# Performance work log

Hardware: AMD Instinct MI355X
Metric: run time of the kernel (lower is better)

Reference implementation:

```python
import jax, jax.numpy as jnp
import numpy as np

H = 16  # heads
K_POLY = 3  # K from init


def setup_inputs() -> dict:
    key = jax.random.key(0)
    ks = jax.random.split(key, 6)
    B, N, D = 4, 1024, 1024
    s = 1.0 / np.sqrt(D)
    return {
        "x": jax.random.normal(ks[0], (B, N, D), jnp.float32),
        "Wq": jax.random.normal(ks[1], (D, D), jnp.float32) * s,
        "bq": jnp.zeros((D,), jnp.float32),
        "Wk": jax.random.normal(ks[2], (D, D), jnp.float32) * s,
        "bk": jnp.zeros((D,), jnp.float32),
        "Wv": jax.random.normal(ks[3], (D, D), jnp.float32) * s,
        "bv": jnp.zeros((D,), jnp.float32),
        "Wo": jax.random.normal(ks[4], (D, D), jnp.float32) * s,
        "bo": jnp.zeros((D,), jnp.float32),
        "w0": jnp.zeros((H,), jnp.float32),
        "w1": jnp.ones((H,), jnp.float32),
        "wK": jnp.zeros((H,), jnp.float32),
    }


def reference(x, Wq, bq, Wk, bk, Wv, bv, Wo, bo, w0, w1, wK):
    B, N, D = x.shape
    d = D // H
    # projections -> [B, H, N, d]
    def proj(W, b):
        return (x @ W + b).reshape(B, N, H, d).transpose(0, 2, 1, 3)
    q = proj(Wq, bq)
    k = proj(Wk, bk)
    v = proj(Wv, bv)
    att = jax.nn.softmax(jnp.einsum('bhnd,bhmd->bhnm', q, k) / jnp.sqrt(jnp.float32(d)), axis=-1)
    att2 = jnp.einsum('bhnm,bhmk->bhnk', att, att)  # att @ att
    attK = att + (K_POLY - 1) * (att2 - att)
    eye = jnp.eye(N, dtype=x.dtype)  # [N, N]
    gf = (w0[None, :, None, None] * eye[None, None]
          + w1[None, :, None, None] * att
          + wK[None, :, None, None] * attK)
    out = jnp.einsum('bhnm,bhmd->bhnd', gf, v)  # [B, H, N, d]
    out = out.transpose(0, 2, 1, 3).reshape(B, N, D)
    return out @ Wo + bo
```

## Files before the change

kernel.cpp:

```cpp
#include <hip/hip_runtime.h>

typedef unsigned short u16;
typedef unsigned int u32;
typedef __attribute__((ext_vector_type(8))) short short8;
typedef __attribute__((ext_vector_type(4))) float f32x4;

__device__ __forceinline__ u16 f2bf(float f) {
  union { float f; u32 u; } c; c.f = f;
  u32 u = c.u;
  u += 0x7fffu + ((u >> 16) & 1u);
  return (u16)(u >> 16);
}
__device__ __forceinline__ float bf2f(u16 h) {
  union { u32 u; float f; } c; c.u = ((u32)h) << 16;
  return c.f;
}

#define GLDS16(g, l)                                                          \
  __builtin_amdgcn_global_load_lds(                                           \
      (const __attribute__((address_space(1))) u32*)(g),                      \
      (__attribute__((address_space(3))) u32*)(l), 16, 0, 0)

#define EXP_SCALE 0.18033688011112042f

__global__ __launch_bounds__(256) void k_cast_x(const float* __restrict__ x,
                                                u16* __restrict__ xb) {
  int i = blockIdx.x * 256 + threadIdx.x;
  float4 v = ((const float4*)x)[i];
  short4 s;
  s.x = (short)f2bf(v.x); s.y = (short)f2bf(v.y);
  s.z = (short)f2bf(v.z); s.w = (short)f2bf(v.w);
  *(short4*)(xb + (size_t)i * 4) = s;
}

__global__ __launch_bounds__(256) void k_trans_w(
    const float* __restrict__ W0, const float* __restrict__ W1,
    const float* __restrict__ W2, const float* __restrict__ W3,
    u16* __restrict__ T0, u16* __restrict__ T1, u16* __restrict__ T2,
    u16* __restrict__ T3) {
  const float* W = blockIdx.z == 0 ? W0 : blockIdx.z == 1 ? W1 : blockIdx.z == 2 ? W2 : W3;
  u16* T = blockIdx.z == 0 ? T0 : blockIdx.z == 1 ? T1 : blockIdx.z == 2 ? T2 : T3;
  __shared__ float tile[32][33];
  int r0 = blockIdx.y * 32, c0 = blockIdx.x * 32;
  int tid = threadIdx.x;
  for (int i = tid; i < 1024; i += 256) {
    int r = i >> 5, c = i & 31;
    tile[r][c] = W[(size_t)(r0 + r) * 1024 + c0 + c];
  }
  __syncthreads();
  for (int i = tid; i < 1024; i += 256) {
    int r = i >> 5, c = i & 31;
    T[(size_t)(c0 + r) * 1024 + r0 + c] = f2bf(tile[c][r]);
  }
}

__global__ __launch_bounds__(512, 2) void k_proj(
    const u16* __restrict__ xb, const u16* __restrict__ WqT,
    const u16* __restrict__ WkT, const u16* __restrict__ WvT,
    const float* __restrict__ bq, const float* __restrict__ bk,
    const float* __restrict__ bv, u16* __restrict__ qh, u16* __restrict__ kh,
    u16* __restrict__ vh, u16* __restrict__ vT) {
  __shared__ __align__(16) u16 As[2][256 * 64];
  __shared__ __align__(16) u16 Bs[2][256 * 64];
  const int m0 = blockIdx.x * 256, n0 = blockIdx.y * 256;
  const int which = blockIdx.z;
  const u16* Ag = xb + (size_t)m0 * 1024;
  const u16* Bg = (which == 0 ? WqT : which == 1 ? WkT : WvT) + (size_t)n0 * 1024;
  const float* bias = which == 0 ? bq : which == 1 ? bk : bv;
  const int tid = threadIdx.x, lane = tid & 63, wid = tid >> 6;
  const int wm = wid >> 2, wn = wid & 3, fr = lane & 15, fg = lane >> 4;

  f32x4 acc[8][4];
#pragma unroll
  for (int i = 0; i < 8; ++i)
#pragma unroll
    for (int j = 0; j < 4; ++j) acc[i][j] = f32x4{0.f, 0.f, 0.f, 0.f};

  auto stage = [&](int kt, int buf) {
#pragma unroll
    for (int L = 0; L < 4; ++L) {
      int q = L * 512 + tid;
      int row = q >> 3, c = q & 7;
      int kc = c ^ (row & 7);
      GLDS16(Ag + (size_t)row * 1024 + kt * 64 + kc * 8, &As[buf][q * 8]);
    }
#pragma unroll
    for (int L = 0; L < 4; ++L) {
      int q = L * 512 + tid;
      int row = q >> 3, c = q & 7;
      int kc = c ^ (row & 7);
      GLDS16(Bg + (size_t)row * 1024 + kt * 64 + kc * 8, &Bs[buf][q * 8]);
    }
  };

  stage(0, 0);
  asm volatile("s_waitcnt vmcnt(0)" ::: "memory");
  __builtin_amdgcn_s_barrier();
  asm volatile("" ::: "memory");
  int cur = 0;
  for (int kt = 0; kt < 16; ++kt) {
    if (kt + 1 < 16) stage(kt + 1, cur ^ 1);
    const u16* as = &As[cur][0];
    const u16* bs = &Bs[cur][0];
#pragma unroll
    for (int ks = 0; ks < 2; ++ks) {
      short8 bf_[4];
#pragma unroll
      for (int j = 0; j < 4; ++j) {
        int row = wn * 64 + j * 16 + fr;
        int kk = ks * 4 + fg;
        bf_[j] = *(const short8*)(bs + row * 64 + ((kk ^ (row & 7)) * 8));
      }
#pragma unroll
      for (int mh = 0; mh < 2; ++mh) {
        short8 af_[4];
#pragma unroll
        for (int i = 0; i < 4; ++i) {
          int row = wm * 128 + mh * 64 + i * 16 + fr;
          int kk = ks * 4 + fg;
          af_[i] = *(const short8*)(as + row * 64 + ((kk ^ (row & 7)) * 8));
        }
#pragma unroll
        for (int i = 0; i < 4; ++i)
#pragma unroll
          for (int j = 0; j < 4; ++j)
            acc[mh * 4 + i][j] = __builtin_amdgcn_mfma_f32_16x16x32_bf16(
                af_[i], bf_[j], acc[mh * 4 + i][j], 0, 0, 0);
      }
    }
    asm volatile("s_waitcnt vmcnt(0) lgkmcnt(0)" ::: "memory");
    __builtin_amdgcn_s_barrier();
    asm volatile("" ::: "memory");
    cur ^= 1;
  }
#pragma unroll
  for (int f = 0; f < 8; ++f)
#pragma unroll
    for (int j2 = 0; j2 < 4; ++j2) {
      int n = n0 + wn * 64 + j2 * 16 + fr;
      float bb = bias[n];
      int h = n >> 6, dc = n & 63;
#pragma unroll
      for (int r = 0; r < 4; ++r) {
        int m = m0 + wm * 128 + (f >> 2) * 64 + (f & 3) * 16 + fg * 4 + r;
        int b = m >> 10, nr = m & 1023;
        int z = b * 16 + h;
        float val = acc[f][j2][r] + bb;
        u16 bv16 = f2bf(val);
        if (which == 0) {
          qh[((size_t)z * 1024 + nr) * 64 + dc] = bv16;
        } else if (which == 1) {
          kh[((size_t)z * 1024 + nr) * 64 + dc] = bv16;
        } else {
          vh[((size_t)z * 1024 + nr) * 64 + dc] = bv16;
          vT[((size_t)z * 64 + dc) * 1024 + nr] = bv16;
        }
      }
    }
}

__device__ __forceinline__ void core128x64_p3(const u16* __restrict__ A,
                                              const u16* __restrict__ Bt, int K,
                                              f32x4 (&acc)[2][4], u16* As,
                                              u16* Bs) {
  const int tid = threadIdx.x;
  const int lane = tid & 63;
  const int w = tid >> 6;
  const int fr = lane & 15, fg = lane >> 4;
  const int sr = tid >> 2, sc = (tid & 3) * 8;
#pragma unroll
  for (int i = 0; i < 2; ++i)
#pragma unroll
    for (int j = 0; j < 4; ++j) acc[i][j] = f32x4{0.f, 0.f, 0.f, 0.f};

  auto stage = [&](int t, int slot) {
    u16* as = As + slot * 4096;
    u16* bs = Bs + slot * 2048;
    const int k0 = t * 32 + sc;
    GLDS16(A + (size_t)sr * K + k0, as + tid * 8);
    GLDS16(A + (size_t)(sr + 64) * K + k0, as + (256 + tid) * 8);
    GLDS16(Bt + (size_t)sr * K + k0, bs + tid * 8);
  };
  auto compute = [&](int slot) {
    const u16* as = As + slot * 4096;
    const u16* bs = Bs + slot * 2048;
    short8 af[2], bfv[4];
#pragma unroll
    for (int i = 0; i < 2; ++i)
      af[i] = *(const short8*)(as + (w * 32 + i * 16 + fr) * 32 + fg * 8);
#pragma unroll
    for (int j = 0; j < 4; ++j)
      bfv[j] = *(const short8*)(bs + (j * 16 + fr) * 32 + fg * 8);
#pragma unroll
    for (int i = 0; i < 2; ++i)
#pragma unroll
      for (int j = 0; j < 4; ++j)
        acc[i][j] = __builtin_amdgcn_mfma_f32_16x16x32_bf16(af[i], bfv[j],
                                                            acc[i][j], 0, 0, 0);
  };

  const int NS = K / 32;
  stage(0, 0);
  stage(1, 1);
  int cs = 0, ss = 2;
  for (int t = 0; t + 2 < NS; ++t) {
    asm volatile("s_waitcnt vmcnt(3) lgkmcnt(0)" ::: "memory");
    __builtin_amdgcn_s_barrier();
    asm volatile("" ::: "memory");
    stage(t + 2, ss);
    compute(cs);
    cs = cs == 2 ? 0 : cs + 1;
    ss = ss == 2 ? 0 : ss + 1;
  }
  asm volatile("s_waitcnt vmcnt(3) lgkmcnt(0)" ::: "memory");
  __builtin_amdgcn_s_barrier();
  asm volatile("" ::: "memory");
  compute(cs);
  cs = cs == 2 ? 0 : cs + 1;
  asm volatile("s_waitcnt vmcnt(0) lgkmcnt(0)" ::: "memory");
  __builtin_amdgcn_s_barrier();
  asm volatile("" ::: "memory");
  compute(cs);
}

__global__ __launch_bounds__(256) void k_pass1(
    const u16* __restrict__ qh, const u16* __restrict__ kh,
    const u16* __restrict__ vT, u16* __restrict__ P1T,
    u16* __restrict__ P1h, float* __restrict__ mlinv) {
  __shared__ __align__(16) u16 Ks[64 * 64];
  __shared__ __align__(16) u16 Vs[64 * 64];
  __shared__ __align__(16) u16 Ps[4][16 * 64];
  const int li = blockIdx.x + 16 * blockIdx.y;
  const int cx = li & 7, jb = li >> 3;
  const int z = cx * 8 + (jb >> 4);
  const int m0 = (jb & 15) * 64;
  const int tid = threadIdx.x, lane = tid & 63, w = tid >> 6;
  const int fr = lane & 15, fg = lane >> 4;
  const int row0 = m0 + w * 16;
  const u16* qbase = qh + (size_t)z * 65536;
  const u16* kbase = kh + (size_t)z * 65536;
  const u16* vbase = vT + (size_t)z * 65536;
  u16* myP = &Ps[w][0];

  short8 qf[2];
#pragma unroll
  for (int kc = 0; kc < 2; ++kc)
    qf[kc] = *(const short8*)(qbase + (size_t)(row0 + fr) * 64 + (kc * 4 + fg) * 8);

  f32x4 o[4];
  float rs[4];
#pragma unroll
  for (int ct = 0; ct < 4; ++ct) o[ct] = f32x4{0.f, 0.f, 0.f, 0.f};
#pragma unroll
  for (int r = 0; r < 4; ++r) rs[r] = 0.f;

  for (int t = 0; t < 16; ++t) {
    const int kv0 = t * 64;
#pragma unroll
    for (int it = 0; it < 2; ++it) {
      int idx = it * 256 + tid;
      int row = idx >> 3, cc = idx & 7;
      GLDS16(kbase + (size_t)(kv0 + row) * 64 + ((cc ^ (row & 7)) * 8),
             Ks + idx * 8);
      GLDS16(vbase + (size_t)row * 1024 + kv0 + ((cc ^ (row & 7)) * 8),
             Vs + idx * 8);
    }
    __syncthreads();
#pragma unroll
    for (int ct = 0; ct < 4; ++ct) {
      int krow = ct * 16 + fr;
      short8 k0 = *(const short8*)(Ks + krow * 64 + ((fg ^ (krow & 7)) * 8));
      short8 k1 = *(const short8*)(Ks + krow * 64 + (((4 + fg) ^ (krow & 7)) * 8));
      f32x4 s = __builtin_amdgcn_mfma_f32_16x16x32_bf16(
          qf[0], k0, f32x4{0.f, 0.f, 0.f, 0.f}, 0, 0, 0);
      s = __builtin_amdgcn_mfma_f32_16x16x32_bf16(qf[1], k1, s, 0, 0, 0);
      int pcol = ct * 16 + fr;
      int cc = pcol >> 3;
#pragma unroll
      for (int r = 0; r < 4; ++r) {
        float e = __builtin_exp2f(s[r] * EXP_SCALE);
        rs[r] += e;
        int prow = fg * 4 + r;
        myP[prow * 64 + ((cc ^ (prow & 7)) * 8) + (pcol & 7)] = f2bf(e);
      }
    }
    asm volatile("s_waitcnt lgkmcnt(0)" ::: "memory");
    short8 p0 = *(const short8*)(myP + fr * 64 + ((fg ^ (fr & 7)) * 8));
    short8 p1 = *(const short8*)(myP + fr * 64 + (((4 + fg) ^ (fr & 7)) * 8));
#pragma unroll
    for (int ct = 0; ct < 4; ++ct) {
      int vrow = ct * 16 + fr;
      short8 v0 = *(const short8*)(Vs + vrow * 64 + ((fg ^ (vrow & 7)) * 8));
      short8 v1 = *(const short8*)(Vs + vrow * 64 + (((4 + fg) ^ (vrow & 7)) * 8));
      o[ct] = __builtin_amdgcn_mfma_f32_16x16x32_bf16(p0, v0, o[ct], 0, 0, 0);
      o[ct] = __builtin_amdgcn_mfma_f32_16x16x32_bf16(p1, v1, o[ct], 0, 0, 0);
    }
    __syncthreads();
  }
#pragma unroll
  for (int off = 1; off < 16; off <<= 1)
#pragma unroll
    for (int r = 0; r < 4; ++r) rs[r] += __shfl_xor(rs[r], off, 64);
  float linv[4];
#pragma unroll
  for (int r = 0; r < 4; ++r) linv[r] = 1.f / rs[r];
#pragma unroll
  for (int ct = 0; ct < 4; ++ct) {
    union { u16 u[4]; short4 s4; } pk;
#pragma unroll
    for (int r = 0; r < 4; ++r) {
      u16 b_ = f2bf(o[ct][r] * linv[r]);
      pk.u[r] = b_;
      myP[(fg * 4 + r) * 64 + ct * 16 + fr] = b_;
    }
    *(short4*)(P1T + ((size_t)z * 64 + ct * 16 + fr) * 1024 + row0 + fg * 4) =
        pk.s4;
  }
  asm volatile("s_waitcnt lgkmcnt(0)" ::: "memory");
  {
    int r_ = lane >> 2;
#pragma unroll
    for (int ch2 = 0; ch2 < 2; ++ch2) {
      int ch = (lane & 3) * 2 + ch2;
      int4 vv = *(const int4*)(myP + r_ * 64 + ch * 8);
      *(int4*)(P1h + ((size_t)z * 1024 + row0 + r_) * 64 + ch * 8) = vv;
    }
  }
  if (fr == 0) {
#pragma unroll
    for (int r = 0; r < 4; ++r)
      mlinv[(size_t)z * 1024 + row0 + fg * 4 + r] = linv[r];
  }
}

__global__ __launch_bounds__(256) void k_pass2(
    const u16* __restrict__ qh, const u16* __restrict__ kh,
    const u16* __restrict__ P1T, const u16* __restrict__ vh,
    const u16* __restrict__ P1h, const float* __restrict__ mlinv,
    const float* __restrict__ w0, const float* __restrict__ w1,
    const float* __restrict__ wK, u16* __restrict__ OH) {
  __shared__ __align__(16) u16 Ks[64 * 64];
  __shared__ __align__(16) u16 Ts[64 * 64];
  __shared__ __align__(16) u16 Ps[4][16 * 64];
  const int li = blockIdx.x + 16 * blockIdx.y;
  const int cx = li & 7, jb = li >> 3;
  const int z = cx * 8 + (jb >> 4);
  const int m0 = (jb & 15) * 64;
  const int tid = threadIdx.x, lane = tid & 63, w = tid >> 6;
  const int fr = lane & 15, fg = lane >> 4;
  const int row0 = m0 + w * 16;
  const int h = z & 15, b = z >> 4;
  const float cw0 = w0[h], cw1 = w1[h] - wK[h], cw2 = 2.f * wK[h];
  const u16* qbase = qh + (size_t)z * 65536;
  const u16* kbase = kh + (size_t)z * 65536;
  const u16* tbase = P1T + (size_t)z * 65536;
  u16* myP = &Ps[w][0];

  short8 qf[2];
#pragma unroll
  for (int kc = 0; kc < 2; ++kc)
    qf[kc] = *(const short8*)(qbase + (size_t)(row0 + fr) * 64 + (kc * 4 + fg) * 8);
  float lrow[4];
#pragma unroll
  for (int r = 0; r < 4; ++r)
    lrow[r] = mlinv[(size_t)z * 1024 + row0 + fg * 4 + r];
  f32x4 o[4];
#pragma unroll
  for (int ct = 0; ct < 4; ++ct) o[ct] = f32x4{0.f, 0.f, 0.f, 0.f};

  for (int t = 0; t < 16; ++t) {
    const int kv0 = t * 64;
#pragma unroll
    for (int it = 0; it < 2; ++it) {
      int idx = it * 256 + tid;
      int row = idx >> 3, cc = idx & 7;
      GLDS16(kbase + (size_t)(kv0 + row) * 64 + ((cc ^ (row & 7)) * 8),
             Ks + idx * 8);
      GLDS16(tbase + (size_t)row * 1024 + kv0 + ((cc ^ (row & 7)) * 8),
             Ts + idx * 8);
    }
    __syncthreads();
#pragma unroll
    for (int ct = 0; ct < 4; ++ct) {
      int krow = ct * 16 + fr;
      short8 k0 = *(const short8*)(Ks + krow * 64 + ((fg ^ (krow & 7)) * 8));
      short8 k1 = *(const short8*)(Ks + krow * 64 + (((4 + fg) ^ (krow & 7)) * 8));
      f32x4 s = __builtin_amdgcn_mfma_f32_16x16x32_bf16(
          qf[0], k0, f32x4{0.f, 0.f, 0.f, 0.f}, 0, 0, 0);
      s = __builtin_amdgcn_mfma_f32_16x16x32_bf16(qf[1], k1, s, 0, 0, 0);
      int pcol = ct * 16 + fr;
      int cc = pcol >> 3;
#pragma unroll
      for (int r = 0; r < 4; ++r) {
        float p = __builtin_exp2f(s[r] * EXP_SCALE) * lrow[r];
        int prow = fg * 4 + r;
        myP[prow * 64 + ((cc ^ (prow & 7)) * 8) + (pcol & 7)] = f2bf(p);
      }
    }
    asm volatile("s_waitcnt lgkmcnt(0)" ::: "memory");
    short8 p0 = *(const short8*)(myP + fr * 64 + ((fg ^ (fr & 7)) * 8));
    short8 p1 = *(const short8*)(myP + fr * 64 + (((4 + fg) ^ (fr & 7)) * 8));
#pragma unroll
    for (int ct = 0; ct < 4; ++ct) {
      int vrow = ct * 16 + fr;
      short8 v0 = *(const short8*)(Ts + vrow * 64 + ((fg ^ (vrow & 7)) * 8));
      short8 v1 = *(const short8*)(Ts + vrow * 64 + (((4 + fg) ^ (vrow & 7)) * 8));
      o[ct] = __builtin_amdgcn_mfma_f32_16x16x32_bf16(p0, v0, o[ct], 0, 0, 0);
      o[ct] = __builtin_amdgcn_mfma_f32_16x16x32_bf16(p1, v1, o[ct], 0, 0, 0);
    }
    __syncthreads();
  }
#pragma unroll
  for (int ct = 0; ct < 4; ++ct)
#pragma unroll
    for (int r = 0; r < 4; ++r)
      myP[(fg * 4 + r) * 64 + ct * 16 + fr] = f2bf(o[ct][r]);
  asm volatile("s_waitcnt lgkmcnt(0)" ::: "memory");
  {
    int r_ = lane >> 2;
    const u16* vp = vh + ((size_t)z * 1024 + row0 + r_) * 64;
    const u16* pp = P1h + ((size_t)z * 1024 + row0 + r_) * 64;
    u16* op = OH + ((size_t)b * 1024 + row0 + r_) * 1024 + h * 64;
#pragma unroll
    for (int ch2 = 0; ch2 < 2; ++ch2) {
      int ch = (lane & 3) * 2 + ch2;
      short8 pv = *(const short8*)(myP + r_ * 64 + ch * 8);
      short8 vv = *(const short8*)(vp + ch * 8);
      short8 p1 = *(const short8*)(pp + ch * 8);
      short8 res;
#pragma unroll
      for (int e = 0; e < 8; ++e) {
        float f = cw0 * bf2f((u16)vv[e]) + cw1 * bf2f((u16)p1[e]) +
                  cw2 * bf2f((u16)pv[e]);
        res[e] = (short)f2bf(f);
      }
      *(short8*)(op + ch * 8) = res;
    }
  }
}

__global__ __launch_bounds__(256) void k_final(const u16* __restrict__ OH,
                                               const u16* __restrict__ WoT,
                                               const float* __restrict__ bo,
                                               float* __restrict__ out) {
  __shared__ __align__(16) u16 As[3 * 128 * 32];
  __shared__ __align__(16) u16 Bs[3 * 64 * 32];
  const int li = blockIdx.x + 32 * blockIdx.y;
  const int cx = li & 7, jb = li >> 3;
  const int m0 = (cx * 4 + (jb & 3)) * 128;
  const int n0 = (jb >> 2) * 64;
  f32x4 acc[2][4];
  core128x64_p3(OH + (size_t)m0 * 1024, WoT + (size_t)n0 * 1024, 1024, acc, As, Bs);
  const int tid = threadIdx.x, lane = tid & 63, w = tid >> 6;
  const int fr = lane & 15, fg = lane >> 4;
#pragma unroll
  for (int i = 0; i < 2; ++i)
#pragma unroll
    for (int j2 = 0; j2 < 4; ++j2) {
      int n = n0 + j2 * 16 + fr;
      float bb = bo[n];
#pragma unroll
      for (int r = 0; r < 4; ++r) {
        int m = m0 + w * 32 + i * 16 + fg * 4 + r;
        out[(size_t)m * 1024 + n] = acc[i][j2][r] + bb;
      }
    }
}

extern "C" void kernel_launch(void* const* d_in, const int* in_sizes, int n_in,
                              void* d_out, int out_size, void* d_ws,
                              size_t ws_size, hipStream_t stream) {
  const float* x = (const float*)d_in[0];
  const float* Wq = (const float*)d_in[1];
  const float* bq = (const float*)d_in[2];
  const float* Wk = (const float*)d_in[3];
  const float* bk = (const float*)d_in[4];
  const float* Wv = (const float*)d_in[5];
  const float* bv = (const float*)d_in[6];
  const float* Wo = (const float*)d_in[7];
  const float* bo = (const float*)d_in[8];
  const float* w0 = (const float*)d_in[9];
  const float* w1 = (const float*)d_in[10];
  const float* wK = (const float*)d_in[11];
  float* out = (float*)d_out;

  char* ws = (char*)d_ws;
  const size_t MB = 1ull << 20;
  u16* xb  = (u16*)(ws);
  u16* WqT = (u16*)(ws + 8 * MB);
  u16* WkT = (u16*)(ws + 10 * MB);
  u16* WvT = (u16*)(ws + 12 * MB);
  u16* WoT = (u16*)(ws + 14 * MB);
  u16* qh  = (u16*)(ws + 16 * MB);
  u16* kh  = (u16*)(ws + 24 * MB);
  u16* vh  = (u16*)(ws + 32 * MB);
  u16* vT  = (u16*)(ws + 40 * MB);
  u16* P1T = (u16*)(ws + 48 * MB);
  u16* P1h = (u16*)(ws + 56 * MB);
  u16* OH  = (u16*)(ws + 64 * MB);
  float* mlinv = (float*)(ws + 72 * MB);

  hipLaunchKernelGGL(k_cast_x, dim3(4096), dim3(256), 0, stream, x, xb);
  hipLaunchKernelGGL(k_trans_w, dim3(32, 32, 4), dim3(256), 0, stream, Wq, Wk,
                     Wv, Wo, WqT, WkT, WvT, WoT);
  hipLaunchKernelGGL(k_proj, dim3(16, 4, 3), dim3(512), 0, stream, xb, WqT, WkT,
                     WvT, bq, bk, bv, qh, kh, vh, vT);
  hipLaunchKernelGGL(k_pass1, dim3(16, 64), dim3(256), 0, stream, qh, kh, vT,
                     P1T, P1h, mlinv);
  hipLaunchKernelGGL(k_pass2, dim3(16, 64), dim3(256), 0, stream, qh, kh, P1T,
                     vh, P1h, mlinv, w0, w1, wK, OH);
  hipLaunchKernelGGL(k_final, dim3(32, 16), dim3(256), 0, stream, OH, WoT, bo,
                     out);
}
```

Before: 177.6 us.

## Triple-buffer k_proj with BK=32 stages and XCD-aware block remap

Rewrites the QKV projection GEMM main loop to use three LDS slots of 32-wide K tiles, issuing loads two stages ahead and waiting with a partial vmcnt so global loads overlap MFMA work. The XOR swizzle on LDS is dropped because of the narrower rows, which may bring back bank conflicts. The 3D grid is flattened to 192 blocks and remapped so that consecutive blocks on the same XCD share weight and activation tiles, aiming for better L2 reuse. LDS per block shrinks, but there are now more barriers per K step.

```diff
diff --git a/kernel.cpp b/kernel.cpp
--- a/kernel.cpp
+++ b/kernel.cpp
@@ -60,10 +60,15 @@
     const float* __restrict__ bq, const float* __restrict__ bk,
     const float* __restrict__ bv, u16* __restrict__ qh, u16* __restrict__ kh,
     u16* __restrict__ vh, u16* __restrict__ vT) {
-  __shared__ __align__(16) u16 As[2][256 * 64];
-  __shared__ __align__(16) u16 Bs[2][256 * 64];
-  const int m0 = blockIdx.x * 256, n0 = blockIdx.y * 256;
-  const int which = blockIdx.z;
+  __shared__ __align__(16) u16 As[3 * 256 * 32];
+  __shared__ __align__(16) u16 Bs[3 * 256 * 32];
+  const int li = blockIdx.x;
+  const int cx = li & 7, j = li >> 3;
+  const int g = cx * 24 + j;
+  const int which = g >> 6;
+  const int rem = g & 63;
+  const int n0 = (rem >> 4) * 256;
+  const int m0 = (rem & 15) * 256;
   const u16* Ag = xb + (size_t)m0 * 1024;
   const u16* Bg = (which == 0 ? WqT : which == 1 ? WkT : WvT) + (size_t)n0 * 1024;
   const float* bias = which == 0 ? bq : which == 1 ? bk : bv;
@@ -74,65 +79,70 @@
 #pragma unroll
   for (int i = 0; i < 8; ++i)
 #pragma unroll
-    for (int j = 0; j < 4; ++j) acc[i][j] = f32x4{0.f, 0.f, 0.f, 0.f};
-
-  auto stage = [&](int kt, int buf) {
-#pragma unroll
-    for (int L = 0; L < 4; ++L) {
+    for (int jj = 0; jj < 4; ++jj) acc[i][jj] = f32x4{0.f, 0.f, 0.f, 0.f};
+
+  auto stage = [&](int t, int slot) {
+    u16* as = As + slot * 8192;
+    u16* bs = Bs + slot * 8192;
+#pragma unroll
+    for (int L = 0; L < 2; ++L) {
       int q = L * 512 + tid;
-      int row = q >> 3, c = q & 7;
-      int kc = c ^ (row & 7);
-      GLDS16(Ag + (size_t)row * 1024 + kt * 64 + kc * 8, &As[buf][q * 8]);
-    }
-#pragma unroll
-    for (int L = 0; L < 4; ++L) {
+      int row = q >> 2, c = q & 3;
+      GLDS16(Ag + (size_t)row * 1024 + t * 32 + c * 8, as + q * 8);
+    }
+#pragma unroll
+    for (int L = 0; L < 2; ++L) {
       int q = L * 512 + tid;
-      int row = q >> 3, c = q & 7;
-      int kc = c ^ (row & 7);
-      GLDS16(Bg + (size_t)row * 1024 + kt * 64 + kc * 8, &Bs[buf][q * 8]);
+      int row = q >> 2, c = q & 3;
+      GLDS16(Bg + (size_t)row * 1024 + t * 32 + c * 8, bs + q * 8);
     }
   };
-
+  auto compute = [&](int slot) {
+    const u16* as = As + slot * 8192;
+    const u16* bs = Bs + slot * 8192;
+    short8 bf_[4];
+#pragma unroll
+    for (int jj = 0; jj < 4; ++jj) {
+      int row = wn * 64 + jj * 16 + fr;
+      bf_[jj] = *(const short8*)(bs + row * 32 + fg * 8);
+    }
+    short8 af_[8];
+#pragma unroll
+    for (int i = 0; i < 8; ++i) {
+      int row = wm * 128 + i * 16 + fr;
+      af_[i] = *(const short8*)(as + row * 32 + fg * 8);
+    }
+#pragma unroll
+    for (int i = 0; i < 8; ++i)
+#pragma unroll
+      for (int jj = 0; jj < 4; ++jj)
+        acc[i][jj] = __builtin_amdgcn_mfma_f32_16x16x32_bf16(af_[i], bf_[jj],
+                                                             acc[i][jj], 0, 0, 0);
+  };
+
+  const int NS = 32;
   stage(0, 0);
-  asm volatile("s_waitcnt vmcnt(0)" ::: "memory");
+  stage(1, 1);
+  int cs = 0, ss = 2;
+  for (int t = 0; t + 2 < NS; ++t) {
+    asm volatile("s_waitcnt vmcnt(4) lgkmcnt(0)" ::: "memory");
+    __builtin_amdgcn_s_barrier();
+    asm volatile("" ::: "memory");
+    stage(t + 2, ss);
+    compute(cs);
+    cs = cs == 2 ? 0 : cs + 1;
+    ss = ss == 2 ? 0 : ss + 1;
+  }
+  asm volatile("s_waitcnt vmcnt(4) lgkmcnt(0)" ::: "memory");
   __builtin_amdgcn_s_barrier();
   asm volatile("" ::: "memory");
-  int cur = 0;
-  for (int kt = 0; kt < 16; ++kt) {
-    if (kt + 1 < 16) stage(kt + 1, cur ^ 1);
-    const u16* as = &As[cur][0];
-    const u16* bs = &Bs[cur][0];
-#pragma unroll
-    for (int ks = 0; ks < 2; ++ks) {
-      short8 bf_[4];
-#pragma unroll
-      for (int j = 0; j < 4; ++j) {
-        int row = wn * 64 + j * 16 + fr;
-        int kk = ks * 4 + fg;
-        bf_[j] = *(const short8*)(bs + row * 64 + ((kk ^ (row & 7)) * 8));
-      }
-#pragma unroll
-      for (int mh = 0; mh < 2; ++mh) {
-        short8 af_[4];
-#pragma unroll
-        for (int i = 0; i < 4; ++i) {
-          int row = wm * 128 + mh * 64 + i * 16 + fr;
-          int kk = ks * 4 + fg;
-          af_[i] = *(const short8*)(as + row * 64 + ((kk ^ (row & 7)) * 8));
-        }
-#pragma unroll
-        for (int i = 0; i < 4; ++i)
-#pragma unroll
-          for (int j = 0; j < 4; ++j)
-            acc[mh * 4 + i][j] = __builtin_amdgcn_mfma_f32_16x16x32_bf16(
-                af_[i], bf_[j], acc[mh * 4 + i][j], 0, 0, 0);
-      }
-    }
-    asm volatile("s_waitcnt vmcnt(0) lgkmcnt(0)" ::: "memory");
-    __builtin_amdgcn_s_barrier();
-    asm volatile("" ::: "memory");
-    cur ^= 1;
-  }
+  compute(cs);
+  cs = cs == 2 ? 0 : cs + 1;
+  asm volatile("s_waitcnt vmcnt(0) lgkmcnt(0)" ::: "memory");
+  __builtin_amdgcn_s_barrier();
+  asm volatile("" ::: "memory");
+  compute(cs);
+
 #pragma unroll
   for (int f = 0; f < 8; ++f)
 #pragma unroll
@@ -142,7 +152,7 @@
       int h = n >> 6, dc = n & 63;
 #pragma unroll
       for (int r = 0; r < 4; ++r) {
-        int m = m0 + wm * 128 + (f >> 2) * 64 + (f & 3) * 16 + fg * 4 + r;
+        int m = m0 + wm * 128 + f * 16 + fg * 4 + r;
         int b = m >> 10, nr = m & 1023;
         int z = b * 16 + h;
         float val = acc[f][j2][r] + bb;
@@ -503,7 +513,7 @@
   hipLaunchKernelGGL(k_cast_x, dim3(4096), dim3(256), 0, stream, x, xb);
   hipLaunchKernelGGL(k_trans_w, dim3(32, 32, 4), dim3(256), 0, stream, Wq, Wk,
                      Wv, Wo, WqT, WkT, WvT, WoT);
-  hipLaunchKernelGGL(k_proj, dim3(16, 4, 3), dim3(512), 0, stream, xb, WqT, WkT,
+  hipLaunchKernelGGL(k_proj, dim3(192), dim3(512), 0, stream, xb, WqT, WkT,
                      WvT, bq, bk, bv, qh, kh, vh, vT);
   hipLaunchKernelGGL(k_pass1, dim3(16, 64), dim3(256), 0, stream, qh, kh, vT,
                      P1T, P1h, mlinv);
```

After: 186.9 us. +5.2%, slower.
